# Performance work log

Hardware: AMD Instinct MI355X
Metric: run time of the kernel (lower is better)

The kernel has to match this reference:

```python
import jax, jax.numpy as jnp
import numpy as np

B, S, D, H = 2, 2048, 1024, 16
HD = D // H  # head_size = 64


def setup_inputs() -> dict:
    key = jax.random.key(0)
    ks = jax.random.split(key, 11)
    s = 1.0 / np.sqrt(D)
    inp = {
        "q": jax.random.normal(ks[0], (B, S, D), jnp.float32),
        "k": jax.random.normal(ks[1], (B, S, D), jnp.float32),
        "v": jax.random.normal(ks[2], (B, S, D), jnp.float32),
        "Wq": jax.random.normal(ks[3], (D, D), jnp.float32) * s,
        "bq": jax.random.normal(ks[4], (D,), jnp.float32) * s,
        "Wk": jax.random.normal(ks[5], (D, D), jnp.float32) * s,
        "bk": jax.random.normal(ks[6], (D,), jnp.float32) * s,
        "Wv": jax.random.normal(ks[7], (D, D), jnp.float32) * s,
        "bv": jax.random.normal(ks[8], (D,), jnp.float32) * s,
        "Wo": jax.random.normal(ks[9], (D, D), jnp.float32) * s,
        "bo": jax.random.normal(ks[10], (D,), jnp.float32) * s,
    }
    return inp


def reference(q, k, v, Wq, bq, Wk, bk, Wv, bv, Wo, bo):
    # project and split heads: [B,S,D] -> [B,H,S,HD]
    def split_heads(x, W, b):
        y = x @ W.T + b
        return y.reshape(B, S, H, HD).transpose(0, 2, 1, 3)

    qh = split_heads(q, Wq, bq)
    kh = split_heads(k, Wk, bk)
    vh = split_heads(v, Wv, bv)

    scale = 1.0 / jnp.sqrt(jnp.asarray(HD, qh.dtype))
    scores = jnp.einsum("bhqd,bhkd->bhqk", qh, kh) * scale  # [B,H,S,S]
    weights = jax.nn.softmax(scores, axis=-1)
    out = jnp.einsum("bhqk,bhkd->bhqd", weights, vh)  # [B,H,S,HD]
    out = out.transpose(0, 2, 1, 3).reshape(B, S, D)
    return out @ Wo.T + bo
```

## Files before the change

kernel.cpp:

```cpp
#include <hip/hip_runtime.h>

typedef __attribute__((ext_vector_type(4))) float f32x4;
typedef __attribute__((ext_vector_type(8))) short bf16x8;
typedef __attribute__((ext_vector_type(8))) unsigned short u16x8;
typedef __attribute__((ext_vector_type(4))) unsigned short u16x4;
typedef __attribute__((ext_vector_type(4))) unsigned int u32x4;
typedef unsigned short ushort_t;

#define LOG2E 1.4426950408889634f

__device__ inline unsigned short f2bf(float x) {
  union { float f; unsigned int u; } v; v.f = x;
  unsigned int r = v.u + 0x7fffu + ((v.u >> 16) & 1u);
  return (unsigned short)(r >> 16);
}

__device__ inline unsigned cvtpk_bf16(float a, float b) {
  unsigned r;
  asm("v_cvt_pk_bf16_f32 %0, %1, %2" : "=v"(r) : "v"(a), "v"(b));
  return r;
}

__device__ inline void gload_lds16(const void* g, void* l) {
  __builtin_amdgcn_global_load_lds(
      (const __attribute__((address_space(1))) unsigned int*)g,
      (__attribute__((address_space(3))) unsigned int*)l, 16, 0, 0);
}

__device__ inline void cvt_body(const float* __restrict__ src, ushort_t* __restrict__ dst, int i) {
  const f32x4* s = (const f32x4*)src;
  f32x4 a = s[2 * i], b = s[2 * i + 1];
  u16x8 o;
#pragma unroll
  for (int j = 0; j < 4; ++j) { o[j] = f2bf(a[j]); o[4 + j] = f2bf(b[j]); }
  *(u16x8*)(dst + (size_t)i * 8) = o;
}

__global__ __launch_bounds__(256) void cvt_bf16(const float* __restrict__ src,
                                                ushort_t* __restrict__ dst, int n8) {
  int i = blockIdx.x * 256 + threadIdx.x;
  if (i < n8) cvt_body(src, dst, i);
}

__global__ __launch_bounds__(256) void cvt3(const float* __restrict__ a,
                                            const float* __restrict__ b,
                                            const float* __restrict__ c,
                                            ushort_t* __restrict__ dst, int n8) {
  int i = blockIdx.x * 256 + threadIdx.x;
  if (i >= n8) return;
  const float* s = blockIdx.y == 0 ? a : (blockIdx.y == 1 ? b : c);
  cvt_body(s, dst + (size_t)blockIdx.y * n8 * 8, i);
}

__global__ __launch_bounds__(256) void cvt4(const float* __restrict__ a,
                                            const float* __restrict__ b,
                                            const float* __restrict__ c,
                                            const float* __restrict__ d,
                                            ushort_t* __restrict__ dst, int n8) {
  int i = blockIdx.x * 256 + threadIdx.x;
  if (i >= n8) return;
  const float* s = blockIdx.y == 0 ? a : (blockIdx.y == 1 ? b : (blockIdx.y == 2 ? c : d));
  cvt_body(s, dst + (size_t)blockIdx.y * n8 * 8, i);
}

template <typename F>
__device__ inline void gemm_core(const ushort_t* __restrict__ A, const ushort_t* __restrict__ W,
                                 int m0, int n0, ushort_t* As, ushort_t* Bs, F&& mfma_step) {
  constexpr int K = 1024;
  const int tid = threadIdx.x, lane = tid & 63, wid = tid >> 6;
  const int srow = lane >> 2, sp = lane & 3;
  for (int k0 = 0; k0 < K; k0 += 32) {
#pragma unroll
    for (int c = 0; c < 2; ++c) {
      int i = wid * 2 + c;
      int row = i * 16 + srow;
      int s = sp ^ ((row >> 1) & 3);
      gload_lds16(A + (size_t)(m0 + row) * K + k0 + s * 8, &As[i * 512]);
      gload_lds16(W + (size_t)(n0 + row) * K + k0 + s * 8, &Bs[i * 512]);
    }
    __syncthreads();
    mfma_step(As, Bs);
    __syncthreads();
  }
}

__global__ __launch_bounds__(256) void proj_gemm(const ushort_t* __restrict__ Abase, int aStride,
                                                 const ushort_t* __restrict__ Wall, int wStride,
                                                 const float* __restrict__ bq,
                                                 const float* __restrict__ bk,
                                                 const float* __restrict__ bv, float qs,
                                                 ushort_t* __restrict__ outQ,
                                                 ushort_t* __restrict__ outK,
                                                 ushort_t* __restrict__ outV, int zofs) {
  __shared__ __attribute__((aligned(16))) ushort_t As[128 * 32];
  __shared__ __attribute__((aligned(16))) ushort_t Bs[128 * 32];
  const int z = blockIdx.z + zofs;
  const ushort_t* A = Abase + (size_t)z * aStride;
  const ushort_t* W = Wall + (size_t)z * wStride;
  const float* bias = z == 0 ? bq : (z == 1 ? bk : bv);
  const float scale = z == 0 ? qs : 1.0f;
  ushort_t* out = z == 0 ? outQ : (z == 1 ? outK : outV);
  const int mode = z == 2 ? 1 : 0;

  const int tid = threadIdx.x, lane = tid & 63, wid = tid >> 6;
  const int m0 = blockIdx.x * 128, n0 = blockIdx.y * 128;
  const int wm = wid >> 1, wn = wid & 1;
  const int qr = lane & 15, kq = lane >> 4;
  f32x4 acc[4][4] = {};

  gemm_core(A, W, m0, n0, As, Bs, [&](ushort_t* as, ushort_t* bs) {
    bf16x8 a[4], b[4];
#pragma unroll
    for (int f = 0; f < 4; ++f) {
      int ra = wm * 64 + f * 16 + qr;
      a[f] = *(const bf16x8*)&as[ra * 32 + (kq ^ ((ra >> 1) & 3)) * 8];
      int rb = wn * 64 + f * 16 + qr;
      b[f] = *(const bf16x8*)&bs[rb * 32 + (kq ^ ((rb >> 1) & 3)) * 8];
    }
#pragma unroll
    for (int i = 0; i < 4; ++i)
#pragma unroll
      for (int j = 0; j < 4; ++j)
        acc[i][j] = __builtin_amdgcn_mfma_f32_16x16x32_bf16(a[i], b[j], acc[i][j], 0, 0, 0);
  });

  const int cm = m0 + wm * 64, cn = n0 + wn * 64;
#pragma unroll
  for (int fn = 0; fn < 4; ++fn) {
    int n = cn + fn * 16 + qr;
    float bvv = bias[n];
    int h = n >> 6, hd = n & 63;
#pragma unroll
    for (int fm = 0; fm < 4; ++fm) {
      int m = cm + fm * 16 + kq * 4;
      if (mode == 0) {
#pragma unroll
        for (int r = 0; r < 4; ++r) {
          int mm = m + r, b = mm >> 11, s = mm & 2047;
          out[((size_t)(b * 16 + h) * 2048 + s) * 64 + hd] = f2bf((acc[fm][fn][r] + bvv) * scale);
        }
      } else {
        int b = m >> 11, s = m & 2047;
        u16x4 pk;
#pragma unroll
        for (int r = 0; r < 4; ++r) pk[r] = f2bf((acc[fm][fn][r] + bvv) * scale);
        *(u16x4*)&out[((size_t)(b * 16 + h) * 64 + hd) * 2048 + s] = pk;
      }
    }
  }
}

__global__ __launch_bounds__(256) void gemm_out(const ushort_t* __restrict__ A,
                                                const ushort_t* __restrict__ W,
                                                const float* __restrict__ bias,
                                                float* __restrict__ out) {
  __shared__ __attribute__((aligned(16))) ushort_t As[128 * 32];
  __shared__ __attribute__((aligned(16))) ushort_t Bs[128 * 32];
  const int tid = threadIdx.x, lane = tid & 63, wid = tid >> 6;
  const int m0 = blockIdx.x * 128, n0 = blockIdx.y * 128;
  const int wm = wid >> 1, wn = wid & 1;
  const int qr = lane & 15, kq = lane >> 4;
  f32x4 acc[4][4] = {};

  gemm_core(A, W, m0, n0, As, Bs, [&](ushort_t* as, ushort_t* bs) {
    bf16x8 a[4], b[4];
#pragma unroll
    for (int f = 0; f < 4; ++f) {
      int ra = wm * 64 + f * 16 + qr;
      a[f] = *(const bf16x8*)&as[ra * 32 + (kq ^ ((ra >> 1) & 3)) * 8];
      int rb = wn * 64 + f * 16 + qr;
      b[f] = *(const bf16x8*)&bs[rb * 32 + (kq ^ ((rb >> 1) & 3)) * 8];
    }
#pragma unroll
    for (int i = 0; i < 4; ++i)
#pragma unroll
      for (int j = 0; j < 4; ++j)
        acc[i][j] = __builtin_amdgcn_mfma_f32_16x16x32_bf16(a[i], b[j], acc[i][j], 0, 0, 0);
  });

  const int cm = m0 + wm * 64, cn = n0 + wn * 64;
#pragma unroll
  for (int fn = 0; fn < 4; ++fn) {
    int n = cn + fn * 16 + qr;
    float bvv = bias[n];
#pragma unroll
    for (int fm = 0; fm < 4; ++fm) {
      int m = cm + fm * 16 + kq * 4;
#pragma unroll
      for (int r = 0; r < 4; ++r) out[(size_t)(m + r) * 1024 + n] = acc[fm][fn][r] + bvv;
    }
  }
}

__global__ __launch_bounds__(256) void attn_fwd(const ushort_t* __restrict__ Qh,
                                                const ushort_t* __restrict__ Kh,
                                                const ushort_t* __restrict__ Vt,
                                                ushort_t* __restrict__ ctx) {
  constexpr int S = 2048, HD = 64, NT = S / 64;
  __shared__ __attribute__((aligned(16))) ushort_t Ks[2][64 * 64];
  __shared__ __attribute__((aligned(16))) ushort_t Vs[2][64 * 64];

  const int tid = threadIdx.x, lane = tid & 63, wid = tid >> 6;
  const int bh = blockIdx.y, qt = blockIdx.x;
  const size_t head = (size_t)bh * S * HD;
  const ushort_t* Qp = Qh + head;
  const ushort_t* Kp = Kh + head;
  const ushort_t* Vp = Vt + head;

  const int qr = lane & 15, kq = lane >> 4;
  const int q0 = qt * 64 + wid * 16;

  bf16x8 qf[2];
  qf[0] = *(const bf16x8*)&Qp[(size_t)(q0 + qr) * HD + kq * 8];
  qf[1] = *(const bf16x8*)&Qp[(size_t)(q0 + qr) * HD + 32 + kq * 8];

  f32x4 accO[4] = {};
  float mrun = -3e38f, lrun = 0.f;

  const int srow8 = lane >> 3, sp8 = lane & 7;

  for (int t = 0; t < NT; ++t) {
    const int buf = t & 1;
    {
      int kv0 = t == 0 ? 0 : (t + 1) * 64;
      int dbuf = t == 0 ? 0 : buf ^ 1;
      if (t == 0 || t + 1 < NT) {
#pragma unroll
        for (int c = 0; c < 2; ++c) {
          int i = wid * 2 + c;
          int row = i * 8 + srow8;
          int s = sp8 ^ (row & 7);
          gload_lds16(&Kp[(size_t)(kv0 + row) * HD + s * 8], &Ks[dbuf][i * 512]);
          gload_lds16(&Vp[(size_t)row * S + kv0 + s * 8], &Vs[dbuf][i * 512]);
        }
      }
      if (t == 0) {
        __syncthreads();
        if (NT > 1) {
#pragma unroll
          for (int c = 0; c < 2; ++c) {
            int i = wid * 2 + c;
            int row = i * 8 + srow8;
            int s = sp8 ^ (row & 7);
            gload_lds16(&Kp[(size_t)(64 + row) * HD + s * 8], &Ks[1][i * 512]);
            gload_lds16(&Vp[(size_t)row * S + 64 + s * 8], &Vs[1][i * 512]);
          }
        }
      }
    }

    f32x4 sc[4] = {};
    __builtin_amdgcn_s_setprio(1);
#pragma unroll
    for (int fn = 0; fn < 4; ++fn) {
      int rk = fn * 16 + qr;
#pragma unroll
      for (int kh = 0; kh < 2; ++kh) {
        bf16x8 kf = *(const bf16x8*)&Ks[buf][rk * 64 + (((kh * 4 + kq) ^ (rk & 7)) * 8)];
        sc[fn] = __builtin_amdgcn_mfma_f32_16x16x32_bf16(kf, qf[kh], sc[fn], 0, 0, 0);
      }
    }
    __builtin_amdgcn_s_setprio(0);

    float t0 = fmaxf(fmaxf(fmaxf(sc[0][0], sc[0][1]), sc[0][2]), sc[0][3]);
    float t1 = fmaxf(fmaxf(fmaxf(sc[1][0], sc[1][1]), sc[1][2]), sc[1][3]);
    float t2 = fmaxf(fmaxf(fmaxf(sc[2][0], sc[2][1]), sc[2][2]), sc[2][3]);
    float t3 = fmaxf(fmaxf(fmaxf(sc[3][0], sc[3][1]), sc[3][2]), sc[3][3]);
    float pm = fmaxf(fmaxf(t0, t1), fmaxf(t2, t3));
    pm = fmaxf(pm, __shfl_xor(pm, 16, 64));
    pm = fmaxf(pm, __shfl_xor(pm, 32, 64));

    bool need = pm > mrun + 8.0f;
    if (__any(need)) {
      float mn = need ? pm : mrun;
      float sf = __builtin_amdgcn_exp2f(mrun - mn);
      mrun = mn;
#pragma unroll
      for (int f2 = 0; f2 < 4; ++f2) accO[f2] *= sf;
      lrun *= sf;
    }

    float pv[4][4];
    float sum = 0.f;
#pragma unroll
    for (int fn = 0; fn < 4; ++fn)
#pragma unroll
      for (int r = 0; r < 4; ++r) {
        float p = __builtin_amdgcn_exp2f(sc[fn][r] - mrun);
        pv[fn][r] = p;
        sum += p;
      }
    sum += __shfl_xor(sum, 16, 64);
    sum += __shfl_xor(sum, 32, 64);
    lrun += sum;

    unsigned wv[4][2];
#pragma unroll
    for (int fn = 0; fn < 4; ++fn) {
      wv[fn][0] = cvtpk_bf16(pv[fn][0], pv[fn][1]);
      wv[fn][1] = cvtpk_bf16(pv[fn][2], pv[fn][3]);
    }

    __builtin_amdgcn_s_setprio(1);
#pragma unroll
    for (int ks = 0; ks < 2; ++ks) {
      unsigned a0 = wv[2 * ks][0], b0 = wv[2 * ks + 1][0];
      unsigned a1 = wv[2 * ks][1], b1 = wv[2 * ks + 1][1];
      asm volatile("v_permlane32_swap_b32 %0, %1" : "+v"(a0), "+v"(b0));
      asm volatile("v_permlane16_swap_b32 %0, %1" : "+v"(a0), "+v"(b0));
      asm volatile("v_permlane32_swap_b32 %0, %1" : "+v"(a1), "+v"(b1));
      asm volatile("v_permlane16_swap_b32 %0, %1" : "+v"(a1), "+v"(b1));
      u32x4 praw;
      praw[0] = a0; praw[1] = a1; praw[2] = b0; praw[3] = b1;
      bf16x8 pf = __builtin_bit_cast(bf16x8, praw);
#pragma unroll
      for (int f2 = 0; f2 < 4; ++f2) {
        int rv = f2 * 16 + qr;
        bf16x8 vf = *(const bf16x8*)&Vs[buf][rv * 64 + (((ks * 4 + kq) ^ (rv & 7)) * 8)];
        accO[f2] = __builtin_amdgcn_mfma_f32_16x16x32_bf16(vf, pf, accO[f2], 0, 0, 0);
      }
    }
    __builtin_amdgcn_s_setprio(0);
    __syncthreads();
  }

  float inv = 1.0f / lrun;
  const int b = bh >> 4, h = bh & 15;
#pragma unroll
  for (int f2 = 0; f2 < 4; ++f2) {
    u16x4 pk;
#pragma unroll
    for (int r = 0; r < 4; ++r) pk[r] = f2bf(accO[f2][r] * inv);
    int col = h * 64 + f2 * 16 + kq * 4;
    *(u16x4*)&ctx[((size_t)b * 2048 + q0 + qr) * 1024 + col] = pk;
  }
}

extern "C" void kernel_launch(void* const* d_in, const int* in_sizes, int n_in,
                              void* d_out, int out_size, void* d_ws, size_t ws_size,
                              hipStream_t stream) {
  const float* q = (const float*)d_in[0];
  const float* k = (const float*)d_in[1];
  const float* v = (const float*)d_in[2];
  const float* Wq = (const float*)d_in[3];
  const float* bq = (const float*)d_in[4];
  const float* Wk = (const float*)d_in[5];
  const float* bk = (const float*)d_in[6];
  const float* Wv = (const float*)d_in[7];
  const float* bv = (const float*)d_in[8];
  const float* Wo = (const float*)d_in[9];
  const float* bo = (const float*)d_in[10];

  char* ws = (char*)d_ws;
  const size_t MB = 1024 * 1024;
  const int NXE = 4194304;
  const int NWE = 1048576;
  const float qs = 0.125f * LOG2E;
  dim3 gg(32, 8), ga(32, 32);

  if (ws_size >= 56 * MB) {
    ushort_t* Xb = (ushort_t*)(ws);
    ushort_t* Wb = (ushort_t*)(ws + 24 * MB);
    ushort_t* Qh = (ushort_t*)(ws + 32 * MB);
    ushort_t* Kh = (ushort_t*)(ws + 40 * MB);
    ushort_t* Vt = (ushort_t*)(ws + 48 * MB);
    cvt3<<<dim3(2048, 3), 256, 0, stream>>>(q, k, v, Xb, NXE / 8);
    cvt4<<<dim3(512, 4), 256, 0, stream>>>(Wq, Wk, Wv, Wo, Wb, NWE / 8);
    proj_gemm<<<dim3(32, 8, 3), 256, 0, stream>>>(Xb, NXE, Wb, NWE, bq, bk, bv, qs,
                                                  Qh, Kh, Vt, 0);
    attn_fwd<<<ga, 256, 0, stream>>>(Qh, Kh, Vt, Xb);
    gemm_out<<<gg, 256, 0, stream>>>(Xb, Wb + (size_t)3 * NWE, bo, (float*)d_out);
  } else if (ws_size >= 40 * MB) {
    ushort_t* Xb = (ushort_t*)(ws);
    ushort_t* Wb = (ushort_t*)(ws + 8 * MB);
    ushort_t* Qh = (ushort_t*)(ws + 16 * MB);
    ushort_t* Kh = (ushort_t*)(ws + 24 * MB);
    ushort_t* Vt = (ushort_t*)(ws + 32 * MB);
    cvt4<<<dim3(512, 4), 256, 0, stream>>>(Wq, Wk, Wv, Wo, Wb, NWE / 8);
    const float* xs[3] = {q, k, v};
    for (int z = 0; z < 3; ++z) {
      cvt_bf16<<<2048, 256, 0, stream>>>(xs[z], Xb, NXE / 8);
      proj_gemm<<<dim3(32, 8, 1), 256, 0, stream>>>(Xb, 0, Wb, NWE, bq, bk, bv, qs,
                                                    Qh, Kh, Vt, z);
    }
    attn_fwd<<<ga, 256, 0, stream>>>(Qh, Kh, Vt, Xb);
    gemm_out<<<gg, 256, 0, stream>>>(Xb, Wb + (size_t)3 * NWE, bo, (float*)d_out);
  } else {
    ushort_t* Xb = (ushort_t*)(ws);
    ushort_t* Wb = (ushort_t*)(ws + 8 * MB);
    ushort_t* Qh = (ushort_t*)(ws + 10 * MB);
    ushort_t* Kh = (ushort_t*)(ws + 18 * MB);
    ushort_t* Vt = (ushort_t*)(ws + 26 * MB);
    const float* xs[3] = {q, k, v};
    const float* wsrc[3] = {Wq, Wk, Wv};
    for (int z = 0; z < 3; ++z) {
      cvt_bf16<<<2048, 256, 0, stream>>>(xs[z], Xb, NXE / 8);
      cvt_bf16<<<512, 256, 0, stream>>>(wsrc[z], Wb, NWE / 8);
      proj_gemm<<<dim3(32, 8, 1), 256, 0, stream>>>(Xb, 0, Wb, 0, bq, bk, bv, qs,
                                                    Qh, Kh, Vt, z);
    }
    attn_fwd<<<ga, 256, 0, stream>>>(Qh, Kh, Vt, Xb);
    cvt_bf16<<<512, 256, 0, stream>>>(Wo, Wb, NWE / 8);
    gemm_out<<<gg, 256, 0, stream>>>(Xb, Wb, bo, (float*)d_out);
  }
}
```

Measured before the change: 155.0 us.

## Process two 16-row query tiles per wave to reuse K/V fragments

Each wave now handles 32 query rows as two independent 16-row tiles with separate softmax state, so each K and V fragment read from LDS feeds two MFMAs. The block covers 128 query rows and the attention grid is halved along the query axis. This cuts LDS traffic and K/V global loads per query row, but it raises register pressure and halves the number of attention blocks, which may lower occupancy and wave parallelism across the GPU.

New measurement: 156.6 us. No clear change (+1.0%).

```diff
diff --git a/kernel.cpp b/kernel.cpp
--- a/kernel.cpp
+++ b/kernel.cpp
@@ -208,14 +208,18 @@
   const ushort_t* Vp = Vt + head;
 
   const int qr = lane & 15, kq = lane >> 4;
-  const int q0 = qt * 64 + wid * 16;
-
-  bf16x8 qf[2];
-  qf[0] = *(const bf16x8*)&Qp[(size_t)(q0 + qr) * HD + kq * 8];
-  qf[1] = *(const bf16x8*)&Qp[(size_t)(q0 + qr) * HD + 32 + kq * 8];
-
-  f32x4 accO[4] = {};
-  float mrun = -3e38f, lrun = 0.f;
+  const int q0 = qt * 128 + wid * 32;
+
+  bf16x8 qfA[2], qfB[2];
+#pragma unroll
+  for (int kh = 0; kh < 2; ++kh) {
+    qfA[kh] = *(const bf16x8*)&Qp[(size_t)(q0 + qr) * HD + kh * 32 + kq * 8];
+    qfB[kh] = *(const bf16x8*)&Qp[(size_t)(q0 + 16 + qr) * HD + kh * 32 + kq * 8];
+  }
+
+  f32x4 accA[4] = {}, accB[4] = {};
+  float mrunA = -3e38f, lrunA = 0.f;
+  float mrunB = -3e38f, lrunB = 0.f;
 
   const int srow8 = lane >> 3, sp8 = lane & 7;
 
@@ -249,7 +253,7 @@
       }
     }
 
-    f32x4 sc[4] = {};
+    f32x4 scA[4] = {}, scB[4] = {};
     __builtin_amdgcn_s_setprio(1);
 #pragma unroll
     for (int fn = 0; fn < 4; ++fn) {
@@ -257,82 +261,128 @@
 #pragma unroll
       for (int kh = 0; kh < 2; ++kh) {
         bf16x8 kf = *(const bf16x8*)&Ks[buf][rk * 64 + (((kh * 4 + kq) ^ (rk & 7)) * 8)];
-        sc[fn] = __builtin_amdgcn_mfma_f32_16x16x32_bf16(kf, qf[kh], sc[fn], 0, 0, 0);
+        scA[fn] = __builtin_amdgcn_mfma_f32_16x16x32_bf16(kf, qfA[kh], scA[fn], 0, 0, 0);
+        scB[fn] = __builtin_amdgcn_mfma_f32_16x16x32_bf16(kf, qfB[kh], scB[fn], 0, 0, 0);
       }
     }
     __builtin_amdgcn_s_setprio(0);
 
-    float t0 = fmaxf(fmaxf(fmaxf(sc[0][0], sc[0][1]), sc[0][2]), sc[0][3]);
-    float t1 = fmaxf(fmaxf(fmaxf(sc[1][0], sc[1][1]), sc[1][2]), sc[1][3]);
-    float t2 = fmaxf(fmaxf(fmaxf(sc[2][0], sc[2][1]), sc[2][2]), sc[2][3]);
-    float t3 = fmaxf(fmaxf(fmaxf(sc[3][0], sc[3][1]), sc[3][2]), sc[3][3]);
-    float pm = fmaxf(fmaxf(t0, t1), fmaxf(t2, t3));
-    pm = fmaxf(pm, __shfl_xor(pm, 16, 64));
-    pm = fmaxf(pm, __shfl_xor(pm, 32, 64));
-
-    bool need = pm > mrun + 8.0f;
-    if (__any(need)) {
-      float mn = need ? pm : mrun;
-      float sf = __builtin_amdgcn_exp2f(mrun - mn);
-      mrun = mn;
-#pragma unroll
-      for (int f2 = 0; f2 < 4; ++f2) accO[f2] *= sf;
-      lrun *= sf;
-    }
-
-    float pv[4][4];
-    float sum = 0.f;
-#pragma unroll
-    for (int fn = 0; fn < 4; ++fn)
-#pragma unroll
-      for (int r = 0; r < 4; ++r) {
-        float p = __builtin_amdgcn_exp2f(sc[fn][r] - mrun);
-        pv[fn][r] = p;
-        sum += p;
-      }
-    sum += __shfl_xor(sum, 16, 64);
-    sum += __shfl_xor(sum, 32, 64);
-    lrun += sum;
-
-    unsigned wv[4][2];
-#pragma unroll
-    for (int fn = 0; fn < 4; ++fn) {
-      wv[fn][0] = cvtpk_bf16(pv[fn][0], pv[fn][1]);
-      wv[fn][1] = cvtpk_bf16(pv[fn][2], pv[fn][3]);
+    unsigned wvA[4][2], wvB[4][2];
+    {
+      float t0 = fmaxf(fmaxf(fmaxf(scA[0][0], scA[0][1]), scA[0][2]), scA[0][3]);
+      float t1 = fmaxf(fmaxf(fmaxf(scA[1][0], scA[1][1]), scA[1][2]), scA[1][3]);
+      float t2 = fmaxf(fmaxf(fmaxf(scA[2][0], scA[2][1]), scA[2][2]), scA[2][3]);
+      float t3 = fmaxf(fmaxf(fmaxf(scA[3][0], scA[3][1]), scA[3][2]), scA[3][3]);
+      float pm = fmaxf(fmaxf(t0, t1), fmaxf(t2, t3));
+      pm = fmaxf(pm, __shfl_xor(pm, 16, 64));
+      pm = fmaxf(pm, __shfl_xor(pm, 32, 64));
+      bool need = pm > mrunA + 8.0f;
+      if (__any(need)) {
+        float mn = need ? pm : mrunA;
+        float sf = __builtin_amdgcn_exp2f(mrunA - mn);
+        mrunA = mn;
+#pragma unroll
+        for (int f2 = 0; f2 < 4; ++f2) accA[f2] *= sf;
+        lrunA *= sf;
+      }
+      float sum = 0.f;
+#pragma unroll
+      for (int fn = 0; fn < 4; ++fn)
+#pragma unroll
+        for (int r = 0; r < 4; ++r) {
+          float p = __builtin_amdgcn_exp2f(scA[fn][r] - mrunA);
+          scA[fn][r] = p;
+          sum += p;
+        }
+      sum += __shfl_xor(sum, 16, 64);
+      sum += __shfl_xor(sum, 32, 64);
+      lrunA += sum;
+#pragma unroll
+      for (int fn = 0; fn < 4; ++fn) {
+        wvA[fn][0] = cvtpk_bf16(scA[fn][0], scA[fn][1]);
+        wvA[fn][1] = cvtpk_bf16(scA[fn][2], scA[fn][3]);
+      }
+    }
+    {
+      float t0 = fmaxf(fmaxf(fmaxf(scB[0][0], scB[0][1]), scB[0][2]), scB[0][3]);
+      float t1 = fmaxf(fmaxf(fmaxf(scB[1][0], scB[1][1]), scB[1][2]), scB[1][3]);
+      float t2 = fmaxf(fmaxf(fmaxf(scB[2][0], scB[2][1]), scB[2][2]), scB[2][3]);
+      float t3 = fmaxf(fmaxf(fmaxf(scB[3][0], scB[3][1]), scB[3][2]), scB[3][3]);
+      float pm = fmaxf(fmaxf(t0, t1), fmaxf(t2, t3));
+      pm = fmaxf(pm, __shfl_xor(pm, 16, 64));
+      pm = fmaxf(pm, __shfl_xor(pm, 32, 64));
+      bool need = pm > mrunB + 8.0f;
+      if (__any(need)) {
+        float mn = need ? pm : mrunB;
+        float sf = __builtin_amdgcn_exp2f(mrunB - mn);
+        mrunB = mn;
+#pragma unroll
+        for (int f2 = 0; f2 < 4; ++f2) accB[f2] *= sf;
+        lrunB *= sf;
+      }
+      float sum = 0.f;
+#pragma unroll
+      for (int fn = 0; fn < 4; ++fn)
+#pragma unroll
+        for (int r = 0; r < 4; ++r) {
+          float p = __builtin_amdgcn_exp2f(scB[fn][r] - mrunB);
+          scB[fn][r] = p;
+          sum += p;
+        }
+      sum += __shfl_xor(sum, 16, 64);
+      sum += __shfl_xor(sum, 32, 64);
+      lrunB += sum;
+#pragma unroll
+      for (int fn = 0; fn < 4; ++fn) {
+        wvB[fn][0] = cvtpk_bf16(scB[fn][0], scB[fn][1]);
+        wvB[fn][1] = cvtpk_bf16(scB[fn][2], scB[fn][3]);
+      }
     }
 
     __builtin_amdgcn_s_setprio(1);
 #pragma unroll
     for (int ks = 0; ks < 2; ++ks) {
-      unsigned a0 = wv[2 * ks][0], b0 = wv[2 * ks + 1][0];
-      unsigned a1 = wv[2 * ks][1], b1 = wv[2 * ks + 1][1];
+      unsigned a0 = wvA[2 * ks][0], b0 = wvA[2 * ks + 1][0];
+      unsigned a1 = wvA[2 * ks][1], b1 = wvA[2 * ks + 1][1];
       asm volatile("v_permlane32_swap_b32 %0, %1" : "+v"(a0), "+v"(b0));
       asm volatile("v_permlane16_swap_b32 %0, %1" : "+v"(a0), "+v"(b0));
       asm volatile("v_permlane32_swap_b32 %0, %1" : "+v"(a1), "+v"(b1));
       asm volatile("v_permlane16_swap_b32 %0, %1" : "+v"(a1), "+v"(b1));
-      u32x4 praw;
-      praw[0] = a0; praw[1] = a1; praw[2] = b0; praw[3] = b1;
-      bf16x8 pf = __builtin_bit_cast(bf16x8, praw);
+      u32x4 prawA; prawA[0] = a0; prawA[1] = a1; prawA[2] = b0; prawA[3] = b1;
+      bf16x8 pfA = __builtin_bit_cast(bf16x8, prawA);
+      unsigned c0 = wvB[2 * ks][0], d0 = wvB[2 * ks + 1][0];
+      unsigned c1 = wvB[2 * ks][1], d1 = wvB[2 * ks + 1][1];
+      asm volatile("v_permlane32_swap_b32 %0, %1" : "+v"(c0), "+v"(d0));
+      asm volatile("v_permlane16_swap_b32 %0, %1" : "+v"(c0), "+v"(d0));
+      asm volatile("v_permlane32_swap_b32 %0, %1" : "+v"(c1), "+v"(d1));
+      asm volatile("v_permlane16_swap_b32 %0, %1" : "+v"(c1), "+v"(d1));
+      u32x4 prawB; prawB[0] = c0; prawB[1] = c1; prawB[2] = d0; prawB[3] = d1;
+      bf16x8 pfB = __builtin_bit_cast(bf16x8, prawB);
 #pragma unroll
       for (int f2 = 0; f2 < 4; ++f2) {
         int rv = f2 * 16 + qr;
         bf16x8 vf = *(const bf16x8*)&Vs[buf][rv * 64 + (((ks * 4 + kq) ^ (rv & 7)) * 8)];
-        accO[f2] = __builtin_amdgcn_mfma_f32_16x16x32_bf16(vf, pf, accO[f2], 0, 0, 0);
+        accA[f2] = __builtin_amdgcn_mfma_f32_16x16x32_bf16(vf, pfA, accA[f2], 0, 0, 0);
+        accB[f2] = __builtin_amdgcn_mfma_f32_16x16x32_bf16(vf, pfB, accB[f2], 0, 0, 0);
       }
     }
     __builtin_amdgcn_s_setprio(0);
     __syncthreads();
   }
 
-  float inv = 1.0f / lrun;
   const int b = bh >> 4, h = bh & 15;
+  float invA = 1.0f / lrunA, invB = 1.0f / lrunB;
 #pragma unroll
   for (int f2 = 0; f2 < 4; ++f2) {
-    u16x4 pk;
-#pragma unroll
-    for (int r = 0; r < 4; ++r) pk[r] = f2bf(accO[f2][r] * inv);
     int col = h * 64 + f2 * 16 + kq * 4;
-    *(u16x4*)&ctx[((size_t)b * 2048 + q0 + qr) * 1024 + col] = pk;
+    u16x4 pkA, pkB;
+#pragma unroll
+    for (int r = 0; r < 4; ++r) {
+      pkA[r] = f2bf(accA[f2][r] * invA);
+      pkB[r] = f2bf(accB[f2][r] * invB);
+    }
+    *(u16x4*)&ctx[((size_t)b * 2048 + q0 + qr) * 1024 + col] = pkA;
+    *(u16x4*)&ctx[((size_t)b * 2048 + q0 + 16 + qr) * 1024 + col] = pkB;
   }
 }
 
@@ -356,7 +406,7 @@
   const int NXE = 4194304;
   const int NWE = 1048576;
   const float qs = 0.125f * LOG2E;
-  dim3 gg(32, 8), ga(32, 32);
+  dim3 gg(32, 8), ga(16, 32);
 
   if (ws_size >= 56 * MB) {
     ushort_t* Xb = (ushort_t*)(ws);
```
